# Kernel tuning notes

Measured on AMD Instinct MI355X. Metric: run time of the kernel, lower is better.

The kernel has to match this reference:

```python
import jax, jax.numpy as jnp
import numpy as np
from jax import lax

B, T, I, H, O = 128, 512, 256, 512, 256


def setup_inputs() -> dict:
    key = jax.random.key(0)
    ks = jax.random.split(key, 7)
    s_ih = 1.0 / np.sqrt(H)
    return {
        "inputs": jax.random.normal(ks[0], (B, T, I), dtype=jnp.float32),
        "W_ih": jax.random.uniform(ks[1], (H, I), jnp.float32, -s_ih, s_ih),
        "b_ih": jax.random.uniform(ks[2], (H,), jnp.float32, -s_ih, s_ih),
        "W_hh": jax.random.uniform(ks[3], (H, H), jnp.float32, -s_ih, s_ih),
        "b_hh": jax.random.uniform(ks[4], (H,), jnp.float32, -s_ih, s_ih),
        "W_out": jax.random.uniform(ks[5], (O, H), jnp.float32, -s_ih, s_ih),
        "b_out": jax.random.uniform(ks[6], (O,), jnp.float32, -s_ih, s_ih),
        "h0": jnp.zeros((H,), dtype=jnp.float32),
    }


def reference(inputs, W_ih, b_ih, W_hh, b_hh, W_out, b_out, h0):
    # inputs: [B, T, I]; returns readout of last hidden state: [B, O]
    Bsz, Tlen = inputs.shape[0], inputs.shape[1]
    inv_T = jnp.asarray(1.0 / Tlen, dtype=inputs.dtype)
    # Precompute input projection for all timesteps (one big GEMM):
    # x_proj[b,t,h] = inputs @ W_ih.T + b_ih + b_hh
    x_proj = jnp.einsum('bti,hi->bth', inputs, W_ih) + (b_ih + b_hh)
    x_proj_t = jnp.swapaxes(x_proj, 0, 1)  # [T, B, H]

    def step(h, xp):
        # RNNCell: tanh(xp + h @ W_hh.T); residual scaling by 1/T
        h_new = jnp.tanh(xp + h @ W_hh.T) * inv_T + h
        return h_new, None

    h_init = jnp.broadcast_to(h0, (Bsz, h0.shape[0]))
    h_last, _ = lax.scan(step, h_init, x_proj_t)
    return h_last @ W_out.T + b_out
```

## Files before the change

kernel.cpp:

```cpp
#include <hip/hip_runtime.h>
#include <stdint.h>

#define NB 128
#define NT 512
#define NI 256
#define NH 512
#define NO 256

__device__ __forceinline__ uint16_t f2bf(float x) {
  uint32_t u = __float_as_uint(x);
  return (uint16_t)((u + 0x7fffu + ((u >> 16) & 1u)) >> 16);
}
__device__ __forceinline__ uint32_t pack2bf(float a, float b) {
  return (uint32_t)f2bf(a) | ((uint32_t)f2bf(b) << 16);
}

#if __has_builtin(__builtin_amdgcn_fdot2_f32_bf16)
typedef __bf16 bf16x2_t __attribute__((ext_vector_type(2)));
#define HAVE_DOT2 1
#endif

__device__ __forceinline__ float dot2bf(uint32_t w, uint32_t h, float acc) {
#ifdef HAVE_DOT2
  return __builtin_amdgcn_fdot2_f32_bf16(__builtin_bit_cast(bf16x2_t, w),
                                         __builtin_bit_cast(bf16x2_t, h), acc, false);
#else
  float wl = __uint_as_float(w << 16), wh = __uint_as_float(w & 0xffff0000u);
  float hl = __uint_as_float(h << 16), hh = __uint_as_float(h & 0xffff0000u);
  return fmaf(wh, hh, fmaf(wl, hl, acc));
#endif
}

__device__ __forceinline__ float dot4x(uint4 w, uint4 h, float a) {
  a = dot2bf(w.x, h.x, a);
  a = dot2bf(w.y, h.y, a);
  a = dot2bf(w.z, h.z, a);
  a = dot2bf(w.w, h.w, a);
  return a;
}

__global__ __launch_bounds__(256) void prep_kernel(const float* __restrict__ Whh,
                                                   const float* __restrict__ Wout,
                                                   uint4* __restrict__ WQ,
                                                   float* __restrict__ WoT) {
  int idx = blockIdx.x * 256 + threadIdx.x;
  if (idx < 64 * 512) {
    int q = idx >> 9, t = idx & 511;
    int jj = q >> 4, c = q & 15;
    int j = (t & 127) * 4 + jj;
    int k2b = (t >> 7) * 64 + c * 4;
    const float* row = Whh + (size_t)j * NH + 2 * k2b;
    float4 f0 = *(const float4*)row;
    float4 f1 = *(const float4*)(row + 4);
    uint4 w;
    w.x = pack2bf(f0.x, f0.y);
    w.y = pack2bf(f0.z, f0.w);
    w.z = pack2bf(f1.x, f1.y);
    w.w = pack2bf(f1.z, f1.w);
    WQ[idx] = w;
  } else {
    int i = idx - 64 * 512;
    int o = i & (NO - 1);
    int k = i >> 8;
    WoT[(size_t)k * NO + o] = Wout[(size_t)o * NH + k];
  }
}

#define BM 128
#define BN 128
#define BK 16
__global__ __launch_bounds__(256) void xproj_kernel(const float* __restrict__ A,
                                                    const float* __restrict__ Wih,
                                                    const float* __restrict__ bih,
                                                    const float* __restrict__ bhh,
                                                    uint16_t* __restrict__ XP) {
  __shared__ float As[BK][BM + 4];
  __shared__ float Bs[BK][BN + 4];
  const int tid = threadIdx.x;
  const int m0 = blockIdx.x * BM;
  const int n0 = blockIdx.y * BN;
  const int lrow = tid >> 2;
  const int lk = (tid & 3) * 4;
  const int tx = tid & 15;
  const int ty = tid >> 4;
  float acc[8][8] = {};

  for (int k0 = 0; k0 < NI; k0 += BK) {
    float4 a0 = *(const float4*)&A[(size_t)(m0 + lrow) * NI + k0 + lk];
    float4 a1 = *(const float4*)&A[(size_t)(m0 + lrow + 64) * NI + k0 + lk];
    float4 b0 = *(const float4*)&Wih[(size_t)(n0 + lrow) * NI + k0 + lk];
    float4 b1 = *(const float4*)&Wih[(size_t)(n0 + lrow + 64) * NI + k0 + lk];
    __syncthreads();
    As[lk + 0][lrow] = a0.x; As[lk + 1][lrow] = a0.y; As[lk + 2][lrow] = a0.z; As[lk + 3][lrow] = a0.w;
    As[lk + 0][lrow + 64] = a1.x; As[lk + 1][lrow + 64] = a1.y; As[lk + 2][lrow + 64] = a1.z; As[lk + 3][lrow + 64] = a1.w;
    Bs[lk + 0][lrow] = b0.x; Bs[lk + 1][lrow] = b0.y; Bs[lk + 2][lrow] = b0.z; Bs[lk + 3][lrow] = b0.w;
    Bs[lk + 0][lrow + 64] = b1.x; Bs[lk + 1][lrow + 64] = b1.y; Bs[lk + 2][lrow + 64] = b1.z; Bs[lk + 3][lrow + 64] = b1.w;
    __syncthreads();
#pragma unroll
    for (int kk = 0; kk < BK; ++kk) {
      float4 av0 = *(const float4*)&As[kk][ty * 8];
      float4 av1 = *(const float4*)&As[kk][ty * 8 + 4];
      float4 bv0 = *(const float4*)&Bs[kk][tx * 8];
      float4 bv1 = *(const float4*)&Bs[kk][tx * 8 + 4];
      float am[8] = {av0.x, av0.y, av0.z, av0.w, av1.x, av1.y, av1.z, av1.w};
      float bn_[8] = {bv0.x, bv0.y, bv0.z, bv0.w, bv1.x, bv1.y, bv1.z, bv1.w};
#pragma unroll
      for (int r = 0; r < 8; ++r)
#pragma unroll
        for (int c = 0; c < 8; ++c) acc[r][c] = fmaf(am[r], bn_[c], acc[r][c]);
    }
  }

  float bias[8];
#pragma unroll
  for (int c = 0; c < 8; ++c) bias[c] = bih[n0 + tx * 8 + c] + bhh[n0 + tx * 8 + c];
#pragma unroll
  for (int r = 0; r < 8; ++r) {
    int m = m0 + ty * 8 + r;
    uint4 w;
    w.x = pack2bf(acc[r][0] + bias[0], acc[r][1] + bias[1]);
    w.y = pack2bf(acc[r][2] + bias[2], acc[r][3] + bias[3]);
    w.z = pack2bf(acc[r][4] + bias[4], acc[r][5] + bias[5]);
    w.w = pack2bf(acc[r][6] + bias[6], acc[r][7] + bias[7]);
    *(uint4*)&XP[(size_t)m * NH + n0 + tx * 8] = w;
  }
}

__global__ __launch_bounds__(512, 2) void recur_kernel(const uint4* __restrict__ WQ,
                                                       const float* __restrict__ WoT,
                                                       const uint16_t* __restrict__ XP,
                                                       const float* __restrict__ h0,
                                                       const float* __restrict__ bout,
                                                       float* __restrict__ out) {
  __shared__ uint4 WL[12][512];
  __shared__ __align__(16) uint16_t h2[2][NH];
  __shared__ float P[4][NH];
  __shared__ float hsf[NH];
  const int t = threadIdx.x;
  const int b = blockIdx.x;
  const int kq = t >> 7;
  const int jb = (t & 127) * 4;
  const float invT = 1.0f / (float)NT;

  uint4 Wr[52];
#pragma unroll
  for (int q = 0; q < 52; ++q) Wr[q] = WQ[q * 512 + t];
#pragma unroll
  for (int c = 0; c < 12; ++c) WL[c][t] = WQ[(52 + c) * 512 + t];

  float hj = h0[t];
  h2[0][t] = f2bf(hj);
  __syncthreads();

  const uint16_t* xpb = XP + (size_t)b * NT * NH;

  for (int ts = 0; ts < NT; ++ts) {
    const int cur = ts & 1;
    float xpj = __uint_as_float((uint32_t)xpb[(size_t)ts * NH + t] << 16);

    const uint32_t* hw = (const uint32_t*)h2[cur];
    float a0 = 0.f, a1 = 0.f, a2 = 0.f, a3 = 0.f;
#pragma unroll
    for (int c = 0; c < 16; ++c) {
      uint4 hv = *(const uint4*)(hw + kq * 64 + c * 4);
      a0 = dot4x(Wr[c], hv, a0);
      a1 = dot4x(Wr[16 + c], hv, a1);
      a2 = dot4x(Wr[32 + c], hv, a2);
      uint4 w3 = (c < 4) ? Wr[48 + c] : WL[c - 4][t];
      a3 = dot4x(w3, hv, a3);
    }
    *(float4*)&P[kq][jb] = make_float4(a0, a1, a2, a3);
    __syncthreads();

    float y = (P[0][t] + P[1][t]) + (P[2][t] + P[3][t]);
    float hnew = fmaf(tanhf(xpj + y), invT, hj);
    hj = hnew;
    h2[cur ^ 1][t] = f2bf(hnew);
    __syncthreads();
  }

  hsf[t] = hj;
  __syncthreads();

  if (t < NO) {
    float c0 = 0.f, c1 = 0.f;
#pragma unroll 4
    for (int k = 0; k < NH; k += 2) {
      c0 = fmaf(WoT[(size_t)k * NO + t], hsf[k], c0);
      c1 = fmaf(WoT[(size_t)(k + 1) * NO + t], hsf[k + 1], c1);
    }
    out[(size_t)b * NO + t] = c0 + c1 + bout[t];
  }
}

extern "C" void kernel_launch(void* const* d_in, const int* in_sizes, int n_in,
                              void* d_out, int out_size, void* d_ws, size_t ws_size,
                              hipStream_t stream) {
  const float* inputs = (const float*)d_in[0];
  const float* Wih    = (const float*)d_in[1];
  const float* bih    = (const float*)d_in[2];
  const float* Whh    = (const float*)d_in[3];
  const float* bhh    = (const float*)d_in[4];
  const float* Wout   = (const float*)d_in[5];
  const float* bout   = (const float*)d_in[6];
  const float* h0     = (const float*)d_in[7];
  float* out = (float*)d_out;

  char* ws = (char*)d_ws;
  uint4*    WQ  = (uint4*)ws;
  float*    WoT = (float*)(ws + (512u << 10));
  uint16_t* XP  = (uint16_t*)(ws + (1u << 20));

  hipLaunchKernelGGL(prep_kernel, dim3(640), dim3(256), 0, stream, Whh, Wout, WQ, WoT);
  hipLaunchKernelGGL(xproj_kernel, dim3(NB * NT / BM, NH / BN), dim3(256), 0, stream,
                     inputs, Wih, bih, bhh, XP);
  hipLaunchKernelGGL(recur_kernel, dim3(NB), dim3(512), 0, stream,
                     WQ, WoT, XP, h0, bout, out);
}
```

Before: 1.006 ms.

## Use bf16 MFMA for input projection, 8-way split recurrence, fast tanh

Replaces the FP32 SIMT tiled GEMM for the input projection with a bf16 MFMA kernel. W_ih is pre-converted to bf16 in the prep kernel along with the summed biases and a vectorized W_out transpose. The recurrent kernel now splits the K dimension 8 ways with 8 outputs per thread, software-prefetches h and LDS weights, and uses an exp/rcp tanh approximation. The aims are faster projection GEMM and shorter per-step latency, at the cost of extra bf16 rounding of the inputs and an approximate tanh.

```diff
diff --git a/kernel.cpp b/kernel.cpp
--- a/kernel.cpp
+++ b/kernel.cpp
@@ -39,16 +39,33 @@
   return a;
 }
 
+__device__ __forceinline__ float fast_tanh(float x) {
+  float e = __expf(2.0f * x);
+#if __has_builtin(__builtin_amdgcn_rcpf)
+  return 1.0f - 2.0f * __builtin_amdgcn_rcpf(e + 1.0f);
+#else
+  return 1.0f - 2.0f / (e + 1.0f);
+#endif
+}
+
+typedef __bf16 bf16x8 __attribute__((ext_vector_type(8)));
+typedef float f32x4 __attribute__((ext_vector_type(4)));
+
 __global__ __launch_bounds__(256) void prep_kernel(const float* __restrict__ Whh,
+                                                   const float* __restrict__ Wih,
                                                    const float* __restrict__ Wout,
+                                                   const float* __restrict__ bih,
+                                                   const float* __restrict__ bhh,
                                                    uint4* __restrict__ WQ,
-                                                   float* __restrict__ WoT) {
+                                                   float* __restrict__ WoT,
+                                                   uint2* __restrict__ Wihb32,
+                                                   float* __restrict__ BS) {
   int idx = blockIdx.x * 256 + threadIdx.x;
-  if (idx < 64 * 512) {
+  if (idx < 32768) {
     int q = idx >> 9, t = idx & 511;
-    int jj = q >> 4, c = q & 15;
-    int j = (t & 127) * 4 + jj;
-    int k2b = (t >> 7) * 64 + c * 4;
+    int jj = q >> 3, c = q & 7;
+    int j = (t & 63) * 8 + jj;
+    int k2b = (t >> 6) * 32 + c * 4;
     const float* row = Whh + (size_t)j * NH + 2 * k2b;
     float4 f0 = *(const float4*)row;
     float4 f1 = *(const float4*)(row + 4);
@@ -58,71 +75,66 @@
     w.z = pack2bf(f1.x, f1.y);
     w.w = pack2bf(f1.z, f1.w);
     WQ[idx] = w;
-  } else {
-    int i = idx - 64 * 512;
-    int o = i & (NO - 1);
-    int k = i >> 8;
-    WoT[(size_t)k * NO + o] = Wout[(size_t)o * NH + k];
-  }
-}
-
-#define BM 128
-#define BN 128
-#define BK 16
-__global__ __launch_bounds__(256) void xproj_kernel(const float* __restrict__ A,
-                                                    const float* __restrict__ Wih,
-                                                    const float* __restrict__ bih,
-                                                    const float* __restrict__ bhh,
-                                                    uint16_t* __restrict__ XP) {
-  __shared__ float As[BK][BM + 4];
-  __shared__ float Bs[BK][BN + 4];
-  const int tid = threadIdx.x;
-  const int m0 = blockIdx.x * BM;
-  const int n0 = blockIdx.y * BN;
-  const int lrow = tid >> 2;
-  const int lk = (tid & 3) * 4;
-  const int tx = tid & 15;
-  const int ty = tid >> 4;
-  float acc[8][8] = {};
-
-  for (int k0 = 0; k0 < NI; k0 += BK) {
-    float4 a0 = *(const float4*)&A[(size_t)(m0 + lrow) * NI + k0 + lk];
-    float4 a1 = *(const float4*)&A[(size_t)(m0 + lrow + 64) * NI + k0 + lk];
-    float4 b0 = *(const float4*)&Wih[(size_t)(n0 + lrow) * NI + k0 + lk];
-    float4 b1 = *(const float4*)&Wih[(size_t)(n0 + lrow + 64) * NI + k0 + lk];
-    __syncthreads();
-    As[lk + 0][lrow] = a0.x; As[lk + 1][lrow] = a0.y; As[lk + 2][lrow] = a0.z; As[lk + 3][lrow] = a0.w;
-    As[lk + 0][lrow + 64] = a1.x; As[lk + 1][lrow + 64] = a1.y; As[lk + 2][lrow + 64] = a1.z; As[lk + 3][lrow + 64] = a1.w;
-    Bs[lk + 0][lrow] = b0.x; Bs[lk + 1][lrow] = b0.y; Bs[lk + 2][lrow] = b0.z; Bs[lk + 3][lrow] = b0.w;
-    Bs[lk + 0][lrow + 64] = b1.x; Bs[lk + 1][lrow + 64] = b1.y; Bs[lk + 2][lrow + 64] = b1.z; Bs[lk + 3][lrow + 64] = b1.w;
-    __syncthreads();
-#pragma unroll
-    for (int kk = 0; kk < BK; ++kk) {
-      float4 av0 = *(const float4*)&As[kk][ty * 8];
-      float4 av1 = *(const float4*)&As[kk][ty * 8 + 4];
-      float4 bv0 = *(const float4*)&Bs[kk][tx * 8];
-      float4 bv1 = *(const float4*)&Bs[kk][tx * 8 + 4];
-      float am[8] = {av0.x, av0.y, av0.z, av0.w, av1.x, av1.y, av1.z, av1.w};
-      float bn_[8] = {bv0.x, bv0.y, bv0.z, bv0.w, bv1.x, bv1.y, bv1.z, bv1.w};
-#pragma unroll
-      for (int r = 0; r < 8; ++r)
-#pragma unroll
-        for (int c = 0; c < 8; ++c) acc[r][c] = fmaf(am[r], bn_[c], acc[r][c]);
+  } else if (idx < 65536) {
+    int i = idx - 32768;
+    float4 f = *(const float4*)(Wih + (size_t)i * 4);
+    uint2 p;
+    p.x = pack2bf(f.x, f.y);
+    p.y = pack2bf(f.z, f.w);
+    Wihb32[i] = p;
+  } else if (idx < 98304) {
+    int i = idx - 65536;
+    int o4 = (i & 63) * 4;
+    int k = i >> 6;
+    float4 v;
+    v.x = Wout[(size_t)(o4 + 0) * NH + k];
+    v.y = Wout[(size_t)(o4 + 1) * NH + k];
+    v.z = Wout[(size_t)(o4 + 2) * NH + k];
+    v.w = Wout[(size_t)(o4 + 3) * NH + k];
+    *(float4*)&WoT[(size_t)k * NO + o4] = v;
+  } else if (idx < 98816) {
+    int n = idx - 98304;
+    BS[n] = bih[n] + bhh[n];
+  }
+}
+
+__global__ __launch_bounds__(256, 2) void xproj_kernel(const float* __restrict__ A,
+                                                       const uint16_t* __restrict__ Wihb,
+                                                       const float* __restrict__ BS,
+                                                       uint16_t* __restrict__ XP) {
+  const int w = threadIdx.x >> 6;
+  const int l = threadIdx.x & 63;
+  const int sl = l & 15, quad = l >> 4;
+  const int m = blockIdx.x * 64 + w * 16 + sl;
+
+  f32x4 acc[32] = {};
+  const float* arow = A + (size_t)m * NI;
+
+  for (int k0 = 0; k0 < NI; k0 += 32) {
+    float4 f0 = *(const float4*)(arow + k0 + quad * 8);
+    float4 f1 = *(const float4*)(arow + k0 + quad * 8 + 4);
+    uint4 ap;
+    ap.x = pack2bf(f0.x, f0.y);
+    ap.y = pack2bf(f0.z, f0.w);
+    ap.z = pack2bf(f1.x, f1.y);
+    ap.w = pack2bf(f1.z, f1.w);
+    bf16x8 afrag = __builtin_bit_cast(bf16x8, ap);
+#pragma unroll
+    for (int u = 0; u < 32; ++u) {
+      uint4 bp = *(const uint4*)(Wihb + (size_t)(u * 16 + sl) * NI + k0 + quad * 8);
+      acc[u] = __builtin_amdgcn_mfma_f32_16x16x32_bf16(
+          __builtin_bit_cast(bf16x8, bp), afrag, acc[u], 0, 0, 0);
     }
   }
 
-  float bias[8];
-#pragma unroll
-  for (int c = 0; c < 8; ++c) bias[c] = bih[n0 + tx * 8 + c] + bhh[n0 + tx * 8 + c];
-#pragma unroll
-  for (int r = 0; r < 8; ++r) {
-    int m = m0 + ty * 8 + r;
-    uint4 w;
-    w.x = pack2bf(acc[r][0] + bias[0], acc[r][1] + bias[1]);
-    w.y = pack2bf(acc[r][2] + bias[2], acc[r][3] + bias[3]);
-    w.z = pack2bf(acc[r][4] + bias[4], acc[r][5] + bias[5]);
-    w.w = pack2bf(acc[r][6] + bias[6], acc[r][7] + bias[7]);
-    *(uint4*)&XP[(size_t)m * NH + n0 + tx * 8] = w;
+  uint16_t* xrow = XP + (size_t)m * NH;
+#pragma unroll
+  for (int u = 0; u < 32; ++u) {
+    float4 bs = *(const float4*)(BS + u * 16 + quad * 4);
+    uint2 pw;
+    pw.x = pack2bf(acc[u][0] + bs.x, acc[u][1] + bs.y);
+    pw.y = pack2bf(acc[u][2] + bs.z, acc[u][3] + bs.w);
+    *(uint2*)(xrow + u * 16 + quad * 4) = pw;
   }
 }
 
@@ -134,19 +146,19 @@
                                                        float* __restrict__ out) {
   __shared__ uint4 WL[12][512];
   __shared__ __align__(16) uint16_t h2[2][NH];
-  __shared__ float P[4][NH];
+  __shared__ float P[8][NH];
   __shared__ float hsf[NH];
   const int t = threadIdx.x;
   const int b = blockIdx.x;
-  const int kq = t >> 7;
-  const int jb = (t & 127) * 4;
+  const int kq8 = t >> 6;
+  const int jb = (t & 63) * 8;
   const float invT = 1.0f / (float)NT;
 
   uint4 Wr[52];
 #pragma unroll
   for (int q = 0; q < 52; ++q) Wr[q] = WQ[q * 512 + t];
 #pragma unroll
-  for (int c = 0; c < 12; ++c) WL[c][t] = WQ[(52 + c) * 512 + t];
+  for (int i = 0; i < 12; ++i) WL[i][t] = WQ[(52 + i) * 512 + t];
 
   float hj = h0[t];
   h2[0][t] = f2bf(hj);
@@ -158,22 +170,40 @@
     const int cur = ts & 1;
     float xpj = __uint_as_float((uint32_t)xpb[(size_t)ts * NH + t] << 16);
 
-    const uint32_t* hw = (const uint32_t*)h2[cur];
+    const uint32_t* hw = (const uint32_t*)h2[cur] + kq8 * 32;
     float a0 = 0.f, a1 = 0.f, a2 = 0.f, a3 = 0.f;
-#pragma unroll
-    for (int c = 0; c < 16; ++c) {
-      uint4 hv = *(const uint4*)(hw + kq * 64 + c * 4);
+    float a4 = 0.f, a5 = 0.f, a6 = 0.f, a7 = 0.f;
+
+    uint4 hv0 = *(const uint4*)(hw);
+    uint4 hv1 = *(const uint4*)(hw + 4);
+    uint4 w6n = Wr[48];
+    uint4 w7n = WL[4][t];
+#pragma unroll
+    for (int c = 0; c < 8; ++c) {
+      uint4 hv = hv0;
+      hv0 = hv1;
+      if (c < 6) hv1 = *(const uint4*)(hw + (c + 2) * 4);
+      uint4 w6 = w6n, w7 = w7n;
+      if (c < 7) {
+        w6n = (c + 1 < 4) ? Wr[48 + c + 1] : WL[c - 3][t];
+        w7n = WL[5 + c][t];
+      }
       a0 = dot4x(Wr[c], hv, a0);
-      a1 = dot4x(Wr[16 + c], hv, a1);
-      a2 = dot4x(Wr[32 + c], hv, a2);
-      uint4 w3 = (c < 4) ? Wr[48 + c] : WL[c - 4][t];
-      a3 = dot4x(w3, hv, a3);
+      a1 = dot4x(Wr[8 + c], hv, a1);
+      a2 = dot4x(Wr[16 + c], hv, a2);
+      a3 = dot4x(Wr[24 + c], hv, a3);
+      a4 = dot4x(Wr[32 + c], hv, a4);
+      a5 = dot4x(Wr[40 + c], hv, a5);
+      a6 = dot4x(w6, hv, a6);
+      a7 = dot4x(w7, hv, a7);
     }
-    *(float4*)&P[kq][jb] = make_float4(a0, a1, a2, a3);
+    *(float4*)&P[kq8][jb] = make_float4(a0, a1, a2, a3);
+    *(float4*)&P[kq8][jb + 4] = make_float4(a4, a5, a6, a7);
     __syncthreads();
 
-    float y = (P[0][t] + P[1][t]) + (P[2][t] + P[3][t]);
-    float hnew = fmaf(tanhf(xpj + y), invT, hj);
+    float y = ((P[0][t] + P[1][t]) + (P[2][t] + P[3][t])) +
+              ((P[4][t] + P[5][t]) + (P[6][t] + P[7][t]));
+    float hnew = fmaf(fast_tanh(xpj + y), invT, hj);
     hj = hnew;
     h2[cur ^ 1][t] = f2bf(hnew);
     __syncthreads();
@@ -207,13 +237,16 @@
   float* out = (float*)d_out;
 
   char* ws = (char*)d_ws;
-  uint4*    WQ  = (uint4*)ws;
-  float*    WoT = (float*)(ws + (512u << 10));
-  uint16_t* XP  = (uint16_t*)(ws + (1u << 20));
-
-  hipLaunchKernelGGL(prep_kernel, dim3(640), dim3(256), 0, stream, Whh, Wout, WQ, WoT);
-  hipLaunchKernelGGL(xproj_kernel, dim3(NB * NT / BM, NH / BN), dim3(256), 0, stream,
-                     inputs, Wih, bih, bhh, XP);
+  uint4*    WQ     = (uint4*)ws;
+  float*    WoT    = (float*)(ws + (512u << 10));
+  uint2*    Wihb32 = (uint2*)(ws + (1024u << 10));
+  float*    BS     = (float*)(ws + (1280u << 10));
+  uint16_t* XP     = (uint16_t*)(ws + (1536u << 10));
+
+  hipLaunchKernelGGL(prep_kernel, dim3(386), dim3(256), 0, stream,
+                     Whh, Wih, Wout, bih, bhh, WQ, WoT, Wihb32, BS);
+  hipLaunchKernelGGL(xproj_kernel, dim3(NB * NT / 64), dim3(256), 0, stream,
+                     inputs, (const uint16_t*)Wihb32, BS, XP);
   hipLaunchKernelGGL(recur_kernel, dim3(NB), dim3(512), 0, stream,
                      WQ, WoT, XP, h0, bout, out);
 }
```

Result: no change. 998.9 us (-0.7%).
